# Optimization experiments

Hardware: AMD Instinct MI355X
Metric: run time of the kernel (lower is better)

Reference implementation:

```python
import jax, jax.numpy as jnp
import numpy as np

B, C, HW = 32, 512, 4096
NUM_CLASSES = 80


def setup_inputs() -> dict:
    key = jax.random.key(0)
    k1, k2 = jax.random.split(key)
    feats = jax.random.normal(k1, (B, C, HW), dtype=jnp.float32)
    # Conv2d(feat_size, num_classes, 1, bias=False) weight -> [num_classes, feat_size]
    W = jax.random.normal(k2, (NUM_CLASSES, C), dtype=jnp.float32) * (1.0 / np.sqrt(C))
    return {"feats": feats, "W": W}


def reference(feats, W):
    # 1x1 conv == per-pixel matmul: [B,C,HW] x [N,C] -> [B,N,HW]
    att_logits = jnp.einsum('bch,nc->bnh', feats, W)
    att_maps = jax.nn.softmax(att_logits, axis=2)  # softmax over spatial dim HW
    # attention-weighted pooling: [B,N,HW] x [B,HW,C] -> [B,N,C]
    cls_feats = jnp.einsum('bnh,bch->bnc', att_maps, feats)
    return cls_feats
```

## Files before the change

kernel.cpp:

```cpp
#include <hip/hip_runtime.h>

#define B_ 32
#define C_ 512
#define HW_ 4096
#define N_ 80
#define HSPLIT 2

typedef __bf16 bf16x8 __attribute__((ext_vector_type(8)));
typedef __bf16 bf16x4 __attribute__((ext_vector_type(4)));
typedef float f32x4 __attribute__((ext_vector_type(4)));
typedef unsigned short u16x8 __attribute__((ext_vector_type(8)));

__device__ __forceinline__ void gload_lds16(const void* g, void* l) {
  __builtin_amdgcn_global_load_lds((const __attribute__((address_space(1))) void*)g,
                                   (__attribute__((address_space(3))) void*)l, 16, 0, 0);
}

#define VMCNT(n) asm volatile("s_waitcnt vmcnt(" #n ")" ::: "memory")
#define SBAR() asm volatile("s_barrier" ::: "memory")

__global__ __launch_bounds__(256) void k0_wfrag(const float* __restrict__ W,
                                                __bf16* __restrict__ Wfrag) {
  const int t = blockIdx.x * 256 + threadIdx.x;
  if (t >= 16 * 5 * 64) return;
  const int cs = t / 320, rem = t % 320;
  const int nf = rem >> 6, lane = rem & 63;
  const int n = nf * 16 + (lane & 15);
  const int c = cs * 32 + (lane >> 4) * 8;
  const float* wp = W + (size_t)n * C_ + c;
  bf16x8 v;
#pragma unroll
  for (int i = 0; i < 8; ++i) v[i] = (__bf16)wp[i];
  *(bf16x8*)(Wfrag + (size_t)t * 8) = v;
}

__global__ __launch_bounds__(256) void kz_zero(float* __restrict__ denom) {
  const int i = blockIdx.x * 256 + threadIdx.x;
  if (i < B_ * N_) denom[i] = 0.f;
}

#define K1_STAGE(CS, SLOT)                                                      \
  {                                                                             \
    _Pragma("unroll") for (int j = 0; j < 4; ++j) {                             \
      const int d = j * 256 + tid;                                              \
      const int r = d >> 5, p = d & 31;                                         \
      gload_lds16(fb + (size_t)((CS)*32 + r) * HW_ + htile0 + p * 4,            \
                  (char*)tile + (SLOT)*16384 + (j * 256 + wave * 64) * 16);     \
    }                                                                           \
  }

#define K1_WLOAD(W, CS)                                                         \
  {                                                                             \
    _Pragma("unroll") for (int nf = 0; nf < 5; ++nf)                            \
        W[nf] = *(const u16x8*)(Wfrag + ((size_t)((CS)*5 + nf) * 64 + lane) * 8); \
  }

#define K1_COMPUTE(T, WU)                                                       \
  {                                                                             \
    const float* tb = (const float*)((char*)tile + ((T) % 3) * 16384);          \
    bf16x8 afr[2];                                                              \
    _Pragma("unroll") for (int hf = 0; hf < 2; ++hf) {                          \
      const int col = wave * 32 + hf * 16 + l16;                                \
      _Pragma("unroll") for (int i = 0; i < 8; ++i)                             \
          afr[hf][i] = (__bf16)tb[(quad * 8 + i) * 128 + col];                  \
    }                                                                           \
    _Pragma("unroll") for (int nf = 0; nf < 5; ++nf) {                          \
      const bf16x8 bfr = __builtin_bit_cast(bf16x8, WU[nf]);                    \
      acc[0][nf] = __builtin_amdgcn_mfma_f32_16x16x32_bf16(afr[0], bfr, acc[0][nf], 0, 0, 0); \
      acc[1][nf] = __builtin_amdgcn_mfma_f32_16x16x32_bf16(afr[1], bfr, acc[1][nf], 0, 0, 0); \
    }                                                                           \
  }

#define K1_ITER(T, WU, WL)                                                      \
  {                                                                             \
    VMCNT(9); SBAR();                                                           \
    K1_WLOAD(WL, (T) + 1);                                                      \
    if ((T) + 2 < 16) K1_STAGE((T) + 2, ((T) + 2) % 3);                         \
    K1_COMPUTE(T, WU);                                                          \
  }

__global__ __launch_bounds__(256, 3) void k1_logits(const float* __restrict__ feats,
                                                    const __bf16* __restrict__ Wfrag,
                                                    __bf16* __restrict__ E,
                                                    float* __restrict__ denom) {
  __shared__ float tile[3][32 * 128];
  const int tid = threadIdx.x;
  const int lane = tid & 63, wave = tid >> 6;
  const int quad = lane >> 4, l16 = lane & 15;
  const int b = blockIdx.y;
  const int htile0 = blockIdx.x * 128;
  const float* fb = feats + (size_t)b * (C_ * HW_);

  const f32x4 zero = {0.f, 0.f, 0.f, 0.f};
  f32x4 acc[2][5];
#pragma unroll
  for (int hf = 0; hf < 2; ++hf)
#pragma unroll
    for (int nf = 0; nf < 5; ++nf) acc[hf][nf] = zero;

  u16x8 wfA[5], wfB[5];
  K1_STAGE(0, 0);
  K1_WLOAD(wfA, 0);
  K1_STAGE(1, 1);

  for (int t = 0; t < 14; t += 2) {
    K1_ITER(t, wfA, wfB);
    K1_ITER(t + 1, wfB, wfA);
  }
  K1_ITER(14, wfA, wfB);
  VMCNT(5); SBAR();
  K1_COMPUTE(15, wfB);

#pragma unroll
  for (int nf = 0; nf < 5; ++nf) {
    const int n = nf * 16 + l16;
    float s = 0.f;
#pragma unroll
    for (int hf = 0; hf < 2; ++hf) {
      bf16x4 pk;
#pragma unroll
      for (int j = 0; j < 4; ++j) {
        const float e = __expf(acc[hf][nf][j]);
        s += e;
        pk[j] = (__bf16)e;
      }
      const int h = htile0 + wave * 32 + hf * 16 + quad * 4;
      *(bf16x4*)(E + (size_t)(b * N_ + n) * HW_ + h) = pk;
    }
    s += __shfl_xor(s, 16);
    s += __shfl_xor(s, 32);
    if (lane < 16) atomicAdd(denom + b * N_ + nf * 16 + lane, s);
  }
}

#define K3_STAGE(TK, SLOT)                                                      \
  {                                                                             \
    const int h0 = hbeg + (TK)*64;                                              \
    _Pragma("unroll") for (int j = 0; j < 2; ++j) {                             \
      const int d = j * 256 + tid;                                              \
      const int r = d >> 4, p = d & 15;                                         \
      gload_lds16(fb + (size_t)(c0 + r) * HW_ + h0 + ((p ^ (r & 15)) << 2),     \
                  (char*)fA + (SLOT)*8192 + (j * 256 + wave * 64) * 16);        \
    }                                                                           \
    _Pragma("unroll") for (int j = 0; j < 2; ++j) {                             \
      const int d = j * 256 + tid;                                              \
      const int r = d >> 3, p = d & 7;                                          \
      gload_lds16(eb + (size_t)r * HW_ + h0 + ((p ^ (r & 7)) << 3),             \
                  (char*)fB + (SLOT)*10240 + (j * 256 + wave * 64) * 16);       \
    }                                                                           \
    {                                                                           \
      const int d = 512 + (wave & 1) * 64 + lane;                               \
      const int r = d >> 3, p = d & 7;                                          \
      gload_lds16(eb + (size_t)r * HW_ + h0 + ((p ^ (r & 7)) << 3),             \
                  (char*)fB + (SLOT)*10240 + (512 + (wave & 1) * 64) * 16);     \
    }                                                                           \
  }

#define K3_COMPUTE(T)                                                           \
  {                                                                             \
    const float* A = (const float*)((char*)fA + ((T) % 4) * 8192);              \
    const __bf16* Bv = (const __bf16*)((char*)fB + ((T) % 4) * 10240);          \
    _Pragma("unroll") for (int ks = 0; ks < 2; ++ks) {                          \
      const int u0 = (ks * 8 + quad * 2) ^ l16;                                 \
      const int u1 = (ks * 8 + quad * 2 + 1) ^ l16;                             \
      const f32x4 va = *(const f32x4*)&A[rA * 64 + u0 * 4];                     \
      const f32x4 vb = *(const f32x4*)&A[rA * 64 + u1 * 4];                     \
      bf16x8 af;                                                                \
      af[0] = (__bf16)va[0]; af[1] = (__bf16)va[1];                             \
      af[2] = (__bf16)va[2]; af[3] = (__bf16)va[3];                             \
      af[4] = (__bf16)vb[0]; af[5] = (__bf16)vb[1];                             \
      af[6] = (__bf16)vb[2]; af[7] = (__bf16)vb[3];                             \
      _Pragma("unroll") for (int nfl = 0; nfl < 3; ++nfl) {                     \
        if (nfl >= nfcnt) break;                                                \
        const int n = (nfbase + nfl) * 16 + l16;                                \
        const int ub = (ks * 4 + quad) ^ (l16 & 7);                             \
        const u16x8 bv = *(const u16x8*)&Bv[n * 64 + ub * 8];                   \
        const bf16x8 bfr = __builtin_bit_cast(bf16x8, bv);                      \
        acc[nfl] = __builtin_amdgcn_mfma_f32_16x16x32_bf16(af, bfr, acc[nfl], 0, 0, 0); \
      }                                                                         \
    }                                                                           \
  }

__global__ __launch_bounds__(256, 2) void k3_pool(const float* __restrict__ feats,
                                                  const __bf16* __restrict__ E,
                                                  float* __restrict__ part) {
  __shared__ float fA[4][32 * 64];
  __shared__ __bf16 fB[4][80 * 64];
  const int tid = threadIdx.x;
  const int lane = tid & 63, wave = tid >> 6;
  const int quad = lane >> 4, l16 = lane & 15;
  const int cf = wave & 1, ng = wave >> 1;
  const int nfbase = ng ? 3 : 0, nfcnt = ng ? 2 : 3;

  const int wg = blockIdx.x;
  const int nid = (wg & 7) * 128 + (wg >> 3);
  const int hz = nid >> 9, rem = nid & 511, b = rem >> 4, cx = rem & 15;
  const int c0 = cx * 32;
  const int hbeg = hz * (HW_ / HSPLIT);

  const float* fb = feats + (size_t)b * (C_ * HW_);
  const __bf16* eb = E + (size_t)b * N_ * HW_;
  const int rA = cf * 16 + l16;

  const f32x4 zero = {0.f, 0.f, 0.f, 0.f};
  f32x4 acc[3];
#pragma unroll
  for (int i = 0; i < 3; ++i) acc[i] = zero;

  K3_STAGE(0, 0);
  K3_STAGE(1, 1);
  K3_STAGE(2, 2);

  for (int t = 0; t < 29; ++t) {
    VMCNT(10); SBAR();
    K3_STAGE(t + 3, (t + 3) & 3);
    K3_COMPUTE(t);
  }
  VMCNT(10); SBAR(); K3_COMPUTE(29);
  VMCNT(5);  SBAR(); K3_COMPUTE(30);
  VMCNT(0);  SBAR(); K3_COMPUTE(31);

  float* pb = part + (size_t)hz * (B_ * N_ * C_);
#pragma unroll
  for (int nfl = 0; nfl < 3; ++nfl) {
    if (nfl >= nfcnt) break;
    const int n = (nfbase + nfl) * 16 + l16;
    float4 v;
    v.x = acc[nfl][0]; v.y = acc[nfl][1]; v.z = acc[nfl][2]; v.w = acc[nfl][3];
    *(float4*)(pb + (size_t)(b * N_ + n) * C_ + c0 + cf * 16 + quad * 4) = v;
  }
}

__global__ __launch_bounds__(256) void k4_reduce(const float* __restrict__ part,
                                                 const float* __restrict__ denom,
                                                 float* __restrict__ out) {
  const size_t i = ((size_t)blockIdx.x * 256 + threadIdx.x) * 4;
  if (i >= (size_t)B_ * N_ * C_) return;
  float4 s = *(const float4*)(part + i);
#pragma unroll
  for (int hz = 1; hz < HSPLIT; ++hz) {
    const float4 v = *(const float4*)(part + (size_t)hz * (B_ * N_ * C_) + i);
    s.x += v.x; s.y += v.y; s.z += v.z; s.w += v.w;
  }
  const float r = 1.0f / denom[i >> 9];
  s.x *= r; s.y *= r; s.z *= r; s.w *= r;
  *(float4*)(out + i) = s;
}

extern "C" void kernel_launch(void* const* d_in, const int* in_sizes, int n_in,
                              void* d_out, int out_size, void* d_ws, size_t ws_size,
                              hipStream_t stream) {
  (void)in_sizes; (void)n_in; (void)out_size; (void)ws_size;
  const float* feats = (const float*)d_in[0];
  const float* Wm = (const float*)d_in[1];
  float* out = (float*)d_out;

  __bf16* E = (__bf16*)d_ws;
  __bf16* Wfrag = E + (size_t)B_ * N_ * HW_;
  float* part = (float*)(Wfrag + 16 * 5 * 64 * 8);
  float* denom = part + (size_t)HSPLIT * B_ * N_ * C_;

  hipLaunchKernelGGL(k0_wfrag, dim3(20), dim3(256), 0, stream, Wm, Wfrag);
  hipLaunchKernelGGL(kz_zero, dim3(10), dim3(256), 0, stream, denom);
  hipLaunchKernelGGL(k1_logits, dim3(HW_ / 128, B_), dim3(256), 0, stream, feats, Wfrag, E, denom);
  hipLaunchKernelGGL(k3_pool, dim3(1024), dim3(256), 0, stream, feats, E, part);
  const int n4 = (B_ * N_ * C_) / 4;
  hipLaunchKernelGGL(k4_reduce, dim3(n4 / 256), dim3(256), 0, stream, part, denom, out);
}
```

Before: 131.9 us.

## Drop HW split in pooling, fuse normalization into k3, merge zero kernel

Removes the two-way spatial split of the pooling kernel so each workgroup covers the full HW range, which lets it apply the softmax denominator directly and write final output. This eliminates the partial-sum buffer and the separate reduce kernel. It also folds denominator zeroing into the weight-fragment kernel, so there are two fewer launches. The trade-off is half as many workgroups (512 on a 256-CU-class device with 2 blocks/CU occupancy), which may reduce latency hiding and parallelism.

```diff
diff --git a/kernel.cpp b/kernel.cpp
--- a/kernel.cpp
+++ b/kernel.cpp
@@ -4,7 +4,6 @@
 #define C_ 512
 #define HW_ 4096
 #define N_ 80
-#define HSPLIT 2
 
 typedef __bf16 bf16x8 __attribute__((ext_vector_type(8)));
 typedef __bf16 bf16x4 __attribute__((ext_vector_type(4)));
@@ -20,8 +19,10 @@
 #define SBAR() asm volatile("s_barrier" ::: "memory")
 
 __global__ __launch_bounds__(256) void k0_wfrag(const float* __restrict__ W,
-                                                __bf16* __restrict__ Wfrag) {
+                                                __bf16* __restrict__ Wfrag,
+                                                float* __restrict__ denom) {
   const int t = blockIdx.x * 256 + threadIdx.x;
+  if (t < B_ * N_) denom[t] = 0.f;
   if (t >= 16 * 5 * 64) return;
   const int cs = t / 320, rem = t % 320;
   const int nf = rem >> 6, lane = rem & 63;
@@ -32,11 +33,6 @@
 #pragma unroll
   for (int i = 0; i < 8; ++i) v[i] = (__bf16)wp[i];
   *(bf16x8*)(Wfrag + (size_t)t * 8) = v;
-}
-
-__global__ __launch_bounds__(256) void kz_zero(float* __restrict__ denom) {
-  const int i = blockIdx.x * 256 + threadIdx.x;
-  if (i < B_ * N_) denom[i] = 0.f;
 }
 
 #define K1_STAGE(CS, SLOT)                                                      \
@@ -135,7 +131,7 @@
 
 #define K3_STAGE(TK, SLOT)                                                      \
   {                                                                             \
-    const int h0 = hbeg + (TK)*64;                                              \
+    const int h0 = (TK)*64;                                                     \
     _Pragma("unroll") for (int j = 0; j < 2; ++j) {                             \
       const int d = j * 256 + tid;                                              \
       const int r = d >> 4, p = d & 15;                                         \
@@ -183,7 +179,8 @@
 
 __global__ __launch_bounds__(256, 2) void k3_pool(const float* __restrict__ feats,
                                                   const __bf16* __restrict__ E,
-                                                  float* __restrict__ part) {
+                                                  const float* __restrict__ denom,
+                                                  float* __restrict__ out) {
   __shared__ float fA[4][32 * 64];
   __shared__ __bf16 fB[4][80 * 64];
   const int tid = threadIdx.x;
@@ -193,10 +190,9 @@
   const int nfbase = ng ? 3 : 0, nfcnt = ng ? 2 : 3;
 
   const int wg = blockIdx.x;
-  const int nid = (wg & 7) * 128 + (wg >> 3);
-  const int hz = nid >> 9, rem = nid & 511, b = rem >> 4, cx = rem & 15;
+  const int nid = (wg & 7) * 64 + (wg >> 3);
+  const int b = nid >> 4, cx = nid & 15;
   const int c0 = cx * 32;
-  const int hbeg = hz * (HW_ / HSPLIT);
 
   const float* fb = feats + (size_t)b * (C_ * HW_);
   const __bf16* eb = E + (size_t)b * N_ * HW_;
@@ -211,40 +207,25 @@
   K3_STAGE(1, 1);
   K3_STAGE(2, 2);
 
-  for (int t = 0; t < 29; ++t) {
+  for (int t = 0; t < 61; ++t) {
     VMCNT(10); SBAR();
     K3_STAGE(t + 3, (t + 3) & 3);
     K3_COMPUTE(t);
   }
-  VMCNT(10); SBAR(); K3_COMPUTE(29);
-  VMCNT(5);  SBAR(); K3_COMPUTE(30);
-  VMCNT(0);  SBAR(); K3_COMPUTE(31);
-
-  float* pb = part + (size_t)hz * (B_ * N_ * C_);
+  VMCNT(10); SBAR(); K3_COMPUTE(61);
+  VMCNT(5);  SBAR(); K3_COMPUTE(62);
+  VMCNT(0);  SBAR(); K3_COMPUTE(63);
+
 #pragma unroll
   for (int nfl = 0; nfl < 3; ++nfl) {
     if (nfl >= nfcnt) break;
     const int n = (nfbase + nfl) * 16 + l16;
+    const float r = 1.0f / denom[b * N_ + n];
     float4 v;
-    v.x = acc[nfl][0]; v.y = acc[nfl][1]; v.z = acc[nfl][2]; v.w = acc[nfl][3];
-    *(float4*)(pb + (size_t)(b * N_ + n) * C_ + c0 + cf * 16 + quad * 4) = v;
-  }
-}
-
-__global__ __launch_bounds__(256) void k4_reduce(const float* __restrict__ part,
-                                                 const float* __restrict__ denom,
-                                                 float* __restrict__ out) {
-  const size_t i = ((size_t)blockIdx.x * 256 + threadIdx.x) * 4;
-  if (i >= (size_t)B_ * N_ * C_) return;
-  float4 s = *(const float4*)(part + i);
-#pragma unroll
-  for (int hz = 1; hz < HSPLIT; ++hz) {
-    const float4 v = *(const float4*)(part + (size_t)hz * (B_ * N_ * C_) + i);
-    s.x += v.x; s.y += v.y; s.z += v.z; s.w += v.w;
-  }
-  const float r = 1.0f / denom[i >> 9];
-  s.x *= r; s.y *= r; s.z *= r; s.w *= r;
-  *(float4*)(out + i) = s;
+    v.x = acc[nfl][0] * r; v.y = acc[nfl][1] * r;
+    v.z = acc[nfl][2] * r; v.w = acc[nfl][3] * r;
+    *(float4*)(out + (size_t)(b * N_ + n) * C_ + c0 + cf * 16 + quad * 4) = v;
+  }
 }
 
 extern "C" void kernel_launch(void* const* d_in, const int* in_sizes, int n_in,
@@ -257,13 +238,9 @@
 
   __bf16* E = (__bf16*)d_ws;
   __bf16* Wfrag = E + (size_t)B_ * N_ * HW_;
-  float* part = (float*)(Wfrag + 16 * 5 * 64 * 8);
-  float* denom = part + (size_t)HSPLIT * B_ * N_ * C_;
-
-  hipLaunchKernelGGL(k0_wfrag, dim3(20), dim3(256), 0, stream, Wm, Wfrag);
-  hipLaunchKernelGGL(kz_zero, dim3(10), dim3(256), 0, stream, denom);
+  float* denom = (float*)(Wfrag + 16 * 5 * 64 * 8);
+
+  hipLaunchKernelGGL(k0_wfrag, dim3(20), dim3(256), 0, stream, Wm, Wfrag, denom);
   hipLaunchKernelGGL(k1_logits, dim3(HW_ / 128, B_), dim3(256), 0, stream, feats, Wfrag, E, denom);
-  hipLaunchKernelGGL(k3_pool, dim3(1024), dim3(256), 0, stream, feats, E, part);
-  const int n4 = (B_ * N_ * C_) / 4;
-  hipLaunchKernelGGL(k4_reduce, dim3(n4 / 256), dim3(256), 0, stream, part, denom, out);
-}
+  hipLaunchKernelGGL(k3_pool, dim3(512), dim3(256), 0, stream, feats, E, denom, out);
+}
```

New measurement: 122.3 us. 7.3% less time.
